# Kernel tuning notes

Hardware: AMD Instinct MI355X
Metric: run time of the kernel (lower is better)

The kernel has to match this reference:

```python
import jax, jax.numpy as jnp
import numpy as np
import math

B, S, HID = 2, 2048, 1024
NH = 16
HD = HID // NH          # 64
VD = HD // 2            # 32 value dim
TD = HD - VD            # 32 type dim
EPS = 1e-6


def setup_inputs() -> dict:
    key = jax.random.key(0)
    ks = jax.random.split(key, 12)
    std = 1.0 / math.sqrt(HID)
    xav = math.sqrt(6.0 / (TD + TD))
    return {
        "x": jax.random.normal(ks[0], (B, S, HID), dtype=jnp.float32),
        "q_w": jax.random.uniform(ks[1], (HID, HID), jnp.float32, -std, std),
        "q_b": jax.random.uniform(ks[2], (HID,), jnp.float32, -std, std),
        "k_w": jax.random.uniform(ks[3], (HID, HID), jnp.float32, -std, std),
        "k_b": jax.random.uniform(ks[4], (HID,), jnp.float32, -std, std),
        "v_w": jax.random.uniform(ks[5], (HID, HID), jnp.float32, -std, std),
        "v_b": jax.random.uniform(ks[6], (HID,), jnp.float32, -std, std),
        "out_w": jax.random.uniform(ks[7], (HID, HID), jnp.float32, -std, std),
        "out_b": jax.random.uniform(ks[8], (HID,), jnp.float32, -std, std),
        "type_bilinear": jax.random.uniform(ks[9], (NH, TD, TD), jnp.float32, -xav, xav),
        "type_bias": jnp.full((NH,), 2.0, dtype=jnp.float32),
        "mask": jnp.ones((B, S), dtype=jnp.int32),
    }


def reference(x, q_w, q_b, k_w, k_b, v_w, v_b, out_w, out_b, type_bilinear, type_bias, mask):
    # projections: [B,S,HID] -> [B,NH,S,HD]
    def proj(w, b):
        y = jnp.einsum("bsi,io->bso", x, w) + b
        return y.reshape(B, S, NH, HD).transpose(0, 2, 1, 3)

    q = proj(q_w, q_b)
    k = proj(k_w, k_b)
    v = proj(v_w, v_b)

    q_val, q_type = q[..., :VD], q[..., VD:]
    k_val, k_type = k[..., :VD], k[..., VD:]

    # standard value score: [B,NH,S,S]
    val_scores = jnp.einsum("bhqd,bhkd->bhqk", q_val, k_val) / math.sqrt(VD)

    # per-head bilinear type score: q_type @ W_h @ k_type^T + bias_h
    qt = jnp.einsum("bhqd,hde->bhqe", q_type, type_bilinear)
    type_scores = jnp.einsum("bhqe,bhke->bhqk", qt, k_type) + type_bias[None, :, None, None]
    type_unif = jax.nn.sigmoid(type_scores)

    scores = val_scores + jnp.log(type_unif + EPS)

    # mask: [B,S] -> broadcast over heads and query dim (keys masked)
    m = (mask[:, None, None, :] != 0)
    scores = jnp.where(m, scores, -jnp.inf)

    attn = jax.nn.softmax(scores, axis=-1)
    out = jnp.einsum("bhqk,bhkd->bhqd", attn, v)          # [B,NH,S,HD]
    out = out.transpose(0, 2, 1, 3).reshape(B, S, HID)
    return jnp.einsum("bsi,io->bso", out, out_w) + out_b
```

## Files before the change

### kernel.cpp

```cpp
#include <hip/hip_runtime.h>
#include <hip/hip_bf16.h>
#include <math.h>

typedef __attribute__((ext_vector_type(8))) short bf16x8;
typedef __attribute__((ext_vector_type(4))) short bf16x4;
typedef __attribute__((ext_vector_type(4))) float f32x4;
typedef __attribute__((ext_vector_type(4))) int   i32x4;

#define NHh 16
#define Sq  2048
#define HIDq 1024
#define HDq 64
#define LOG2E 1.4426950408889634f

#if __has_builtin(__builtin_amdgcn_exp2f)
#define EXP2F(x) __builtin_amdgcn_exp2f(x)
#else
#define EXP2F(x) exp2f(x)
#endif
#if __has_builtin(__builtin_amdgcn_rcpf)
#define RCPF(x) __builtin_amdgcn_rcpf(x)
#else
#define RCPF(x) (1.0f/(x))
#endif

#if __has_builtin(__builtin_amdgcn_mfma_f32_16x16x16bf16_1k)
__device__ __forceinline__ f32x4 MFMA16(bf16x4 a, bf16x4 b, f32x4 c){
  return __builtin_amdgcn_mfma_f32_16x16x16bf16_1k(a, b, c, 0, 0, 0);
}
#else
__device__ __forceinline__ f32x4 MFMA16(bf16x4 a, bf16x4 b, f32x4 c){
  asm volatile("v_mfma_f32_16x16x16_bf16 %0, %1, %2, %0\n\ts_nop 7\n\ts_nop 7"
               : "+v"(c) : "v"(a), "v"(b));
  return c;
}
#endif

__device__ __forceinline__ unsigned short f2bf(float f){
  union { float f; unsigned u; } v; v.f = f;
  unsigned r = v.u + 0x7fffu + ((v.u >> 16) & 1u);
  return (unsigned short)(r >> 16);
}
__device__ __forceinline__ float bf2f(unsigned short s){
  union { unsigned u; float f; } v; v.u = ((unsigned)s) << 16;
  return v.f;
}
__device__ __forceinline__ unsigned pk2bf(float lo, float hi){
  union { __hip_bfloat162 h; unsigned u; } w;
  w.h = __float22bfloat162_rn(make_float2(lo, hi));
  return w.u;
}

__device__ __forceinline__ void gload_lds16(const unsigned short* g, unsigned short* l){
  __builtin_amdgcn_global_load_lds(
      (const __attribute__((address_space(1))) unsigned int*)g,
      (__attribute__((address_space(3))) unsigned int*)l, 16, 0, 0);
}

__global__ __launch_bounds__(256) void convert_x(const float* __restrict__ in,
                                                 unsigned short* __restrict__ out, int n8,
                                                 const int* __restrict__ mask,
                                                 unsigned short* __restrict__ Mbf){
  int bid = blockIdx.x;
  int nmain = gridDim.x - 2;
  if (bid >= nmain){
    int base = (bid - nmain)*2048 + threadIdx.x*8;
    #pragma unroll
    for (int j=0;j<8;j++) Mbf[base+j] = mask[base+j] ? (unsigned short)0x3F80 : (unsigned short)0;
    return;
  }
  int i = bid*256 + threadIdx.x;
  if (i >= n8) return;
  const f32x4* p = (const f32x4*)(in + (size_t)i*8);
  f32x4 a = p[0], b = p[1];
  union { unsigned short us[8]; i32x4 v; } o;
  #pragma unroll
  for (int j=0;j<4;j++){ o.us[j] = f2bf(a[j]); o.us[4+j] = f2bf(b[j]); }
  *(i32x4*)(out + (size_t)i*8) = o.v;
}

__global__ __launch_bounds__(256) void transpose_w(const float* __restrict__ w0, const float* __restrict__ w1,
                                                   const float* __restrict__ w2, const float* __restrict__ w3,
                                                   unsigned short* __restrict__ wT){
  __shared__ float tile[32][33];
  int z = blockIdx.z;
  const float* w = (z==0)?w0:(z==1)?w1:(z==2)?w2:w3;
  unsigned short* dst = wT + (size_t)z*HIDq*HIDq;
  int tx = threadIdx.x, ty = threadIdx.y;
  int n0 = blockIdx.x*32, k0 = blockIdx.y*32;
  #pragma unroll
  for (int i=ty;i<32;i+=8) tile[i][tx] = w[(size_t)(k0+i)*HIDq + n0+tx];
  __syncthreads();
  #pragma unroll
  for (int i=ty;i<32;i+=8) dst[(size_t)(n0+i)*HIDq + k0+tx] = f2bf(tile[tx][i]);
}

__device__ __forceinline__ void gemm_core_gl(const unsigned short* __restrict__ Ag,
                                             const unsigned short* __restrict__ Bg,
                                             unsigned short* As, unsigned short* Bs,
                                             int t, int wv, int lane, int wr, int wc, int lr, int g,
                                             f32x4 acc[4][4]){
  for (int k0=0; k0<HIDq; k0+=64){
    __syncthreads();
    #pragma unroll
    for (int j=0;j<4;j++){
      int flat = (j*4+wv)*64 + lane;
      int row = flat>>3, c = flat&7;
      int srcc = (c ^ (row&7))*8;
      gload_lds16(Ag + (size_t)row*HIDq + k0 + srcc, &As[flat*8]);
      gload_lds16(Bg + (size_t)row*HIDq + k0 + srcc, &Bs[flat*8]);
    }
    __syncthreads();
    #pragma unroll
    for (int ks=0; ks<2; ks++){
      bf16x8 af[4], bfv[4];
      #pragma unroll
      for (int m=0;m<4;m++){
        int rr = wr + m*16 + lr;
        af[m]  = *(bf16x8*)&As[rr*64 + (((ks*4+g) ^ (rr&7))*8)];
      }
      #pragma unroll
      for (int n=0;n<4;n++){
        int rr = wc + n*16 + lr;
        bfv[n] = *(bf16x8*)&Bs[rr*64 + (((ks*4+g) ^ (rr&7))*8)];
      }
      #pragma unroll
      for (int n=0;n<4;n++)
        #pragma unroll
        for (int m=0;m<4;m++)
          acc[n][m] = __builtin_amdgcn_mfma_f32_16x16x32_bf16(bfv[n], af[m], acc[n][m], 0,0,0);
    }
  }
}

__global__ __launch_bounds__(256) void gemm_qkv(const unsigned short* __restrict__ xbf,
    const unsigned short* __restrict__ wT,
    const float* __restrict__ q_b, const float* __restrict__ k_b, const float* __restrict__ v_b,
    const int* __restrict__ mask,
    unsigned short* __restrict__ Qeff, unsigned short* __restrict__ Keff,
    unsigned short* __restrict__ Vt){
  __shared__ unsigned short As[128*64];
  __shared__ unsigned short Bs[128*64];
  const int t = threadIdx.x;
  const int wv = t>>6, lane = t&63, g = lane>>4, lr = lane&15;
  const int wr = (wv>>1)*64, wc = (wv&1)*64;
  f32x4 acc[4][4] = {};
  const int xb = blockIdx.x, yb = blockIdx.y;
  const float VS = 0.25501335f;

  if (xb < 16){
    const int row0 = yb*128, col0 = xb*128;
    gemm_core_gl(xbf + (size_t)row0*HIDq, wT + (size_t)col0*HIDq, As, Bs, t, wv, lane, wr, wc, lr, g, acc);
    #pragma unroll
    for (int n=0;n<4;n++){
      #pragma unroll
      for (int m=0;m<4;m++){
        int row = row0 + wr + m*16 + lr;
        int b_ = row>>11, ss = row&2047;
        int colb = col0 + wc + n*16 + g*4;
        int seg = colb>>10, cw = colb&1023;
        int hh = cw>>6, d = cw&63;
        const float* bp = seg ? k_b : q_b;
        f32x4 bb = *(const f32x4*)&bp[cw];
        float sc = seg ? 1.0f : (d < 32 ? VS : -LOG2E);
        unsigned short* E = seg ? Keff : Qeff;
        float v0 = (acc[n][m][0]+bb[0])*sc, v1 = (acc[n][m][1]+bb[1])*sc;
        float v2 = (acc[n][m][2]+bb[2])*sc, v3 = (acc[n][m][3]+bb[3])*sc;
        union { unsigned u[2]; unsigned long long ll; } W;
        W.u[0] = pk2bf(v0,v1); W.u[1] = pk2bf(v2,v3);
        *(unsigned long long*)&E[(((size_t)b_*NHh+hh)*Sq+ss)*HDq + d] = W.ll;
      }
    }
  } else {
    const int row0 = (xb-16)*128, col0 = yb*128;
    gemm_core_gl(wT + (size_t)2*HIDq*HIDq + (size_t)row0*HIDq, xbf + (size_t)col0*HIDq,
                 As, Bs, t, wv, lane, wr, wc, lr, g, acc);
    #pragma unroll
    for (int n=0;n<4;n++){
      #pragma unroll
      for (int m=0;m<4;m++){
        int chan = row0 + wr + m*16 + lr;
        int hh = chan>>6, d = chan&63;
        float bv = v_b[chan];
        int colb = col0 + wc + n*16 + g*4;
        int b_ = colb>>11, ss = colb&2047;
        i32x4 mk = *(const i32x4*)&mask[(size_t)b_*Sq + ss];
        float m0 = mk[0]?1.f:0.f, m1 = mk[1]?1.f:0.f, m2 = mk[2]?1.f:0.f, m3 = mk[3]?1.f:0.f;
        union { unsigned u[2]; unsigned long long ll; } W;
        W.u[0] = pk2bf((acc[n][m][0]+bv)*m0, (acc[n][m][1]+bv)*m1);
        W.u[1] = pk2bf((acc[n][m][2]+bv)*m2, (acc[n][m][3]+bv)*m3);
        *(unsigned long long*)&Vt[(((size_t)b_*NHh+hh)*HDq + d)*Sq + ss] = W.ll;
      }
    }
  }
}

__global__ __launch_bounds__(256) void gemm_out(const unsigned short* __restrict__ A,
                                                const unsigned short* __restrict__ Bt,
                                                const float* __restrict__ bias,
                                                float* __restrict__ C){
  __shared__ unsigned short As[128*64];
  __shared__ unsigned short Bs[128*64];
  const int t = threadIdx.x;
  const int wv = t>>6, lane = t&63, g = lane>>4, lr = lane&15;
  const int wr = (wv>>1)*64, wc = (wv&1)*64;
  const int row0 = blockIdx.y*128, col0 = blockIdx.x*128;
  f32x4 acc[4][4] = {};
  gemm_core_gl(A + (size_t)row0*HIDq, Bt + (size_t)col0*HIDq, As, Bs, t, wv, lane, wr, wc, lr, g, acc);
  #pragma unroll
  for (int n=0;n<4;n++){
    #pragma unroll
    for (int m=0;m<4;m++){
      int row = row0 + wr + m*16 + lr;
      int colb = col0 + wc + n*16 + g*4;
      f32x4 bb = *(const f32x4*)&bias[colb];
      f32x4 o = acc[n][m] + bb;
      *(f32x4*)&C[(size_t)row*HIDq + colb] = o;
    }
  }
}

__global__ __launch_bounds__(256,4) void attn_kernel(
    const unsigned short* __restrict__ Qe, const unsigned short* __restrict__ Ke,
    const unsigned short* __restrict__ Vt, const float* __restrict__ Tb,
    const float* __restrict__ tbias, const unsigned short* __restrict__ Mbf,
    unsigned short* __restrict__ Obuf)
{
  __shared__ __align__(16) unsigned char smem[32768];
  unsigned short* Ks0 = (unsigned short*)smem;
  unsigned short* Ks1 = (unsigned short*)(smem + 8192);
  unsigned short* Vs0 = (unsigned short*)(smem + 16384);
  unsigned short* Vs1 = (unsigned short*)(smem + 24576);
  float* qls = (float*)smem;
  unsigned short* qtls = Vs0;

  const int t = threadIdx.x;
  const int dd = blockIdx.x;
  const int slot = dd>>3, xcd = dd&7;
  const int x = slot & 31;
  const int bh = ((slot>>5)<<3) | xcd;
  const int h = bh & 15, b = bh >> 4;
  const int q0 = x*64;
  const int wv = t>>6, lane = t&63, g = lane>>4, lr = lane&15;

  const unsigned short* Qb  = Qe + (((size_t)b*NHh+h)*Sq + q0)*HDq;
  const unsigned short* Kb  = Ke + ((size_t)b*NHh+h)*(size_t)Sq*HDq;
  const unsigned short* Vtb = Vt + ((size_t)b*NHh+h)*(size_t)HDq*Sq;
  const unsigned short* Mbfb = Mbf + (size_t)b*Sq;

  {
    int row = t>>2, c8 = (t&3)*8;
    bf16x8 v = *(const bf16x8*)(Qb + (size_t)row*HDq + 32 + c8);
    #pragma unroll
    for (int j=0;j<8;j++) qls[row*33 + c8 + j] = bf2f((unsigned short)v[j]);
  }
  __syncthreads();
  {
    int row = t&63, e0 = (t>>6)*8;
    const float* Th = Tb + (size_t)h*1024;
    float a[8] = {};
    #pragma unroll 4
    for (int d=0; d<32; d++){
      float qd = qls[row*33 + d];
      const f32x4* tp = (const f32x4*)(Th + d*32 + e0);
      f32x4 t0 = tp[0], t1 = tp[1];
      a[0]+=qd*t0[0]; a[1]+=qd*t0[1]; a[2]+=qd*t0[2]; a[3]+=qd*t0[3];
      a[4]+=qd*t1[0]; a[5]+=qd*t1[1]; a[6]+=qd*t1[2]; a[7]+=qd*t1[3];
    }
    union { unsigned u[2]; unsigned long long ll; } W0, W1;
    W0.u[0]=pk2bf(a[0],a[1]); W0.u[1]=pk2bf(a[2],a[3]);
    W1.u[0]=pk2bf(a[4],a[5]); W1.u[1]=pk2bf(a[6],a[7]);
    *(unsigned long long*)&qtls[row*40 + e0]     = W0.ll;
    *(unsigned long long*)&qtls[row*40 + e0 + 4] = W1.ll;
  }
  bf16x8 qvf = *(const bf16x8*)(Qb + (size_t)(wv*16+lr)*HDq + g*8);
  __syncthreads();
  bf16x8 qtn = *(const bf16x8*)&qtls[(wv*16+lr)*40 + g*8];
  __syncthreads();

  #pragma unroll
  for (int i=0;i<2;i++){
    int c = t + i*256;
    int kr = c>>3, kc = c&7;
    gload_lds16(Kb + (size_t)kr*HDq + ((kc ^ (kr&7))*8), Ks0 + c*8);
    int vd = c>>3, vc = c&7;
    gload_lds16(Vtb + (size_t)vd*Sq + ((vc ^ (vd&7))*8), Vs0 + c*8);
  }
  __syncthreads();

  const float tbn = -tbias[h]*LOG2E;
  const f32x4 tbc = {tbn,tbn,tbn,tbn};
  const f32x4 zf = {0.f,0.f,0.f,0.f};
  f32x4 oT[4] = {};
  f32x4 lsum = {0.f,0.f,0.f,0.f};

  auto phase = [&](const unsigned short* Kc, const unsigned short* Vc, int key0,
                   bool doStage, int key0n, unsigned short* Kn, unsigned short* Vn){
    if (doStage){
      #pragma unroll
      for (int i=0;i<2;i++){
        int c = t + i*256;
        int kr = c>>3, kc = c&7;
        gload_lds16(Kb + (size_t)(key0n+kr)*HDq + ((kc ^ (kr&7))*8), Kn + c*8);
        int vd = c>>3, vc = c&7;
        gload_lds16(Vtb + (size_t)vd*Sq + key0n + ((vc ^ (vd&7))*8), Vn + c*8);
      }
    }
    f32x4 sv[4], st[4];
    __builtin_amdgcn_s_setprio(1);
    #pragma unroll
    for (int ks=0; ks<4; ks++){
      const unsigned short* kb = Kc + (ks*16+lr)*64;
      bf16x8 kf0 = *(const bf16x8*)(kb + (((g  ) ^ (lr&7))*8));
      bf16x8 kf1 = *(const bf16x8*)(kb + (((4+g) ^ (lr&7))*8));
      sv[ks] = __builtin_amdgcn_mfma_f32_16x16x32_bf16(kf0, qvf, zf, 0,0,0);
      st[ks] = __builtin_amdgcn_mfma_f32_16x16x32_bf16(kf1, qtn, tbc, 0,0,0);
    }
    __builtin_amdgcn_s_setprio(0);
    bf16x4 pa[4];
    #pragma unroll
    for (int ks=0; ks<4; ks++){
      float p0 = EXP2F(sv[ks][0]) * RCPF(1.f + EXP2F(st[ks][0]));
      float p1 = EXP2F(sv[ks][1]) * RCPF(1.f + EXP2F(st[ks][1]));
      float p2 = EXP2F(sv[ks][2]) * RCPF(1.f + EXP2F(st[ks][2]));
      float p3 = EXP2F(sv[ks][3]) * RCPF(1.f + EXP2F(st[ks][3]));
      union { unsigned u[2]; bf16x4 v; } P_;
      P_.u[0] = pk2bf(p0,p1); P_.u[1] = pk2bf(p2,p3);
      pa[ks] = P_.v;
    }
    #pragma unroll
    for (int ks=0; ks<4; ks++){
      bf16x4 mfr = *(const bf16x4*)(Mbfb + key0 + ks*16 + g*4);
      __builtin_amdgcn_s_setprio(1);
      lsum = MFMA16(pa[ks], mfr, lsum);
      #pragma unroll
      for (int db=0; db<4; db++){
        bf16x4 vf = *(const bf16x4*)(Vc + (db*16+lr)*64 + (((2*ks + (g>>1)) ^ (lr&7))*8 + 4*(g&1)));
        oT[db] = MFMA16(pa[ks], vf, oT[db]);
      }
      __builtin_amdgcn_s_setprio(0);
    }
  };

  for (int kt=0; kt<Sq; kt+=128){
    phase(Ks0, Vs0, kt,      true,           kt+64,  Ks1, Vs1);
    __syncthreads();
    phase(Ks1, Vs1, kt+64,   kt+128 < Sq,    kt+128, Ks0, Vs0);
    __syncthreads();
  }

  float linv[4];
  #pragma unroll
  for (int r=0;r<4;r++) linv[r] = (lsum[r] > 0.f) ? RCPF(lsum[r]) : 0.f;
  unsigned short* Ob = Obuf + ((size_t)b*Sq + (q0 + wv*16 + g*4))*HIDq + h*HDq + lr;
  #pragma unroll
  for (int db=0; db<4; db++){
    #pragma unroll
    for (int r=0;r<4;r++)
      Ob[(size_t)r*HIDq + db*16] = f2bf(oT[db][r]*linv[r]);
  }
}

extern "C" void kernel_launch(void* const* d_in, const int* in_sizes, int n_in,
                              void* d_out, int out_size, void* d_ws, size_t ws_size,
                              hipStream_t stream) {
  const float* x     = (const float*)d_in[0];
  const float* q_w   = (const float*)d_in[1];
  const float* q_b   = (const float*)d_in[2];
  const float* k_w   = (const float*)d_in[3];
  const float* k_b   = (const float*)d_in[4];
  const float* v_w   = (const float*)d_in[5];
  const float* v_b   = (const float*)d_in[6];
  const float* out_w = (const float*)d_in[7];
  const float* out_b = (const float*)d_in[8];
  const float* Tb    = (const float*)d_in[9];
  const float* tbias = (const float*)d_in[10];
  const int*   mask  = (const int*)d_in[11];

  const size_t MROWS = 4096;
  unsigned short* xbf  = (unsigned short*)d_ws;
  unsigned short* wT   = xbf  + MROWS*HIDq;
  unsigned short* Qeff = wT   + (size_t)4*HIDq*HIDq;
  unsigned short* Keff = Qeff + MROWS*HIDq;
  unsigned short* Vt   = Keff + MROWS*HIDq;
  unsigned short* Obuf = Vt   + MROWS*HIDq;
  unsigned short* Mbf  = Obuf + MROWS*HIDq;

  int n8 = (int)(MROWS*HIDq/8);
  convert_x<<<dim3(n8/256 + 2), dim3(256), 0, stream>>>(x, xbf, n8, mask, Mbf);
  transpose_w<<<dim3(32,32,4), dim3(32,8), 0, stream>>>(q_w, k_w, v_w, out_w, wT);

  gemm_qkv<<<dim3(24,32), dim3(256), 0, stream>>>(xbf, wT, q_b, k_b, v_b, mask, Qeff, Keff, Vt);

  attn_kernel<<<dim3(1024), dim3(256), 0, stream>>>(Qeff, Keff, Vt, Tb, tbias, Mbf, Obuf);

  gemm_out<<<dim3(8,32), dim3(256), 0, stream>>>(Obuf, wT + (size_t)3*HIDq*HIDq, out_b, (float*)d_out);
}
```

Measured before the change: 158.9 us.

## Deepen attention K/V prefetch pipeline and shrink output GEMM tiles

The attention kernel moves from a two-buffer K/V ping-pong to three K buffers and two V buffers. K is prefetched two tiles ahead and V one tile ahead, and each phase waits on an explicit vmcnt with a raw s_barrier instead of full __syncthreads. This is meant to hide global-to-LDS latency behind the MFMA work. Separately, the output GEMM switches to 128x64 tiles with its own inline k-loop, doubling the block count (16x32 grid) so more CUs are busy, at the cost of more A-tile reloads and a single-buffered loop.

```diff
diff --git a/kernel.cpp b/kernel.cpp
--- a/kernel.cpp
+++ b/kernel.cpp
@@ -200,15 +200,51 @@
                                                 const float* __restrict__ bias,
                                                 float* __restrict__ C){
   __shared__ unsigned short As[128*64];
-  __shared__ unsigned short Bs[128*64];
+  __shared__ unsigned short Bs[64*64];
   const int t = threadIdx.x;
   const int wv = t>>6, lane = t&63, g = lane>>4, lr = lane&15;
-  const int wr = (wv>>1)*64, wc = (wv&1)*64;
-  const int row0 = blockIdx.y*128, col0 = blockIdx.x*128;
-  f32x4 acc[4][4] = {};
-  gemm_core_gl(A + (size_t)row0*HIDq, Bt + (size_t)col0*HIDq, As, Bs, t, wv, lane, wr, wc, lr, g, acc);
-  #pragma unroll
-  for (int n=0;n<4;n++){
+  const int wr = (wv>>1)*64, wc = (wv&1)*32;
+  const int row0 = blockIdx.y*128, col0 = blockIdx.x*64;
+  f32x4 acc[2][4] = {};
+  for (int k0=0; k0<HIDq; k0+=64){
+    __syncthreads();
+    #pragma unroll
+    for (int j=0;j<4;j++){
+      int flat = t + j*256;
+      int row = flat>>3, c = flat&7;
+      int srcc = (c ^ (row&7))*8;
+      gload_lds16(A + (size_t)(row0+row)*HIDq + k0 + srcc, &As[flat*8]);
+    }
+    #pragma unroll
+    for (int j=0;j<2;j++){
+      int flat = t + j*256;
+      int row = flat>>3, c = flat&7;
+      int srcc = (c ^ (row&7))*8;
+      gload_lds16(Bt + (size_t)(col0+row)*HIDq + k0 + srcc, &Bs[flat*8]);
+    }
+    __syncthreads();
+    #pragma unroll
+    for (int ks=0; ks<2; ks++){
+      bf16x8 af[4], bfv[2];
+      #pragma unroll
+      for (int m=0;m<4;m++){
+        int rr = wr + m*16 + lr;
+        af[m]  = *(bf16x8*)&As[rr*64 + (((ks*4+g) ^ (rr&7))*8)];
+      }
+      #pragma unroll
+      for (int n=0;n<2;n++){
+        int rr = wc + n*16 + lr;
+        bfv[n] = *(bf16x8*)&Bs[rr*64 + (((ks*4+g) ^ (rr&7))*8)];
+      }
+      #pragma unroll
+      for (int n=0;n<2;n++)
+        #pragma unroll
+        for (int m=0;m<4;m++)
+          acc[n][m] = __builtin_amdgcn_mfma_f32_16x16x32_bf16(bfv[n], af[m], acc[n][m], 0,0,0);
+    }
+  }
+  #pragma unroll
+  for (int n=0;n<2;n++){
     #pragma unroll
     for (int m=0;m<4;m++){
       int row = row0 + wr + m*16 + lr;
@@ -226,13 +262,14 @@
     const float* __restrict__ tbias, const unsigned short* __restrict__ Mbf,
     unsigned short* __restrict__ Obuf)
 {
-  __shared__ __align__(16) unsigned char smem[32768];
-  unsigned short* Ks0 = (unsigned short*)smem;
-  unsigned short* Ks1 = (unsigned short*)(smem + 8192);
-  unsigned short* Vs0 = (unsigned short*)(smem + 16384);
-  unsigned short* Vs1 = (unsigned short*)(smem + 24576);
+  __shared__ __align__(16) unsigned char smem[40960];
+  unsigned short* Kb0 = (unsigned short*)smem;
+  unsigned short* Kb1 = (unsigned short*)(smem + 8192);
+  unsigned short* Kb2 = (unsigned short*)(smem + 16384);
+  unsigned short* Vb0 = (unsigned short*)(smem + 24576);
+  unsigned short* Vb1 = (unsigned short*)(smem + 32768);
   float* qls = (float*)smem;
-  unsigned short* qtls = Vs0;
+  unsigned short* qtls = Vb1;
 
   const int t = threadIdx.x;
   const int dd = blockIdx.x;
@@ -267,6 +304,7 @@
       a[0]+=qd*t0[0]; a[1]+=qd*t0[1]; a[2]+=qd*t0[2]; a[3]+=qd*t0[3];
       a[4]+=qd*t1[0]; a[5]+=qd*t1[1]; a[6]+=qd*t1[2]; a[7]+=qd*t1[3];
     }
+    __syncthreads();
     union { unsigned u[2]; unsigned long long ll; } W0, W1;
     W0.u[0]=pk2bf(a[0],a[1]); W0.u[1]=pk2bf(a[2],a[3]);
     W1.u[0]=pk2bf(a[4],a[5]); W1.u[1]=pk2bf(a[6],a[7]);
@@ -282,9 +320,10 @@
   for (int i=0;i<2;i++){
     int c = t + i*256;
     int kr = c>>3, kc = c&7;
-    gload_lds16(Kb + (size_t)kr*HDq + ((kc ^ (kr&7))*8), Ks0 + c*8);
+    gload_lds16(Kb + (size_t)kr*HDq + ((kc ^ (kr&7))*8), Kb0 + c*8);
     int vd = c>>3, vc = c&7;
-    gload_lds16(Vtb + (size_t)vd*Sq + ((vc ^ (vd&7))*8), Vs0 + c*8);
+    gload_lds16(Vtb + (size_t)vd*Sq + ((vc ^ (vd&7))*8), Vb0 + c*8);
+    gload_lds16(Kb + (size_t)(64+kr)*HDq + ((kc ^ (kr&7))*8), Kb1 + c*8);
   }
   __syncthreads();
 
@@ -295,17 +334,29 @@
   f32x4 lsum = {0.f,0.f,0.f,0.f};
 
   auto phase = [&](const unsigned short* Kc, const unsigned short* Vc, int key0,
-                   bool doStage, int key0n, unsigned short* Kn, unsigned short* Vn){
-    if (doStage){
+                   bool stK, int keyK, unsigned short* Kn,
+                   bool stV, int keyV, unsigned short* Vn, bool vm8){
+    if (stK){
       #pragma unroll
       for (int i=0;i<2;i++){
         int c = t + i*256;
         int kr = c>>3, kc = c&7;
-        gload_lds16(Kb + (size_t)(key0n+kr)*HDq + ((kc ^ (kr&7))*8), Kn + c*8);
+        gload_lds16(Kb + (size_t)(keyK+kr)*HDq + ((kc ^ (kr&7))*8), Kn + c*8);
+      }
+    }
+    if (stV){
+      #pragma unroll
+      for (int i=0;i<2;i++){
+        int c = t + i*256;
         int vd = c>>3, vc = c&7;
-        gload_lds16(Vtb + (size_t)vd*Sq + key0n + ((vc ^ (vd&7))*8), Vn + c*8);
-      }
-    }
+        gload_lds16(Vtb + (size_t)vd*Sq + keyV + ((vc ^ (vd&7))*8), Vn + c*8);
+      }
+    }
+    if (vm8) asm volatile("s_waitcnt vmcnt(8)" ::: "memory");
+    else     asm volatile("s_waitcnt vmcnt(4)" ::: "memory");
+    __builtin_amdgcn_sched_barrier(0);
+    __builtin_amdgcn_s_barrier();
+
     f32x4 sv[4], st[4];
     __builtin_amdgcn_s_setprio(1);
     #pragma unroll
@@ -340,14 +391,20 @@
       }
       __builtin_amdgcn_s_setprio(0);
     }
+    __builtin_amdgcn_s_barrier();
   };
 
-  for (int kt=0; kt<Sq; kt+=128){
-    phase(Ks0, Vs0, kt,      true,           kt+64,  Ks1, Vs1);
-    __syncthreads();
-    phase(Ks1, Vs1, kt+64,   kt+128 < Sq,    kt+128, Ks0, Vs0);
-    __syncthreads();
-  }
+  for (int j=0; j<5; j++){
+    int kt = j*384;
+    phase(Kb0, Vb0, kt,      true, kt+128, Kb2,  true, kt+64,  Vb1, true);
+    phase(Kb1, Vb1, kt+64,   true, kt+192, Kb0,  true, kt+128, Vb0, true);
+    phase(Kb2, Vb0, kt+128,  true, kt+256, Kb1,  true, kt+192, Vb1, true);
+    phase(Kb0, Vb1, kt+192,  true, kt+320, Kb2,  true, kt+256, Vb0, true);
+    phase(Kb1, Vb0, kt+256,  true, kt+384, Kb0,  true, kt+320, Vb1, true);
+    phase(Kb2, Vb1, kt+320,  (kt+448 < Sq), kt+448, Kb1,  true, kt+384, Vb0, true);
+  }
+  phase(Kb0, Vb0, 1920,  false, 0, Kb0,  true, 1984, Vb1, false);
+  phase(Kb1, Vb1, 1984,  false, 0, Kb0,  false, 0, Vb0,  false);
 
   float linv[4];
   #pragma unroll
@@ -394,5 +451,5 @@
 
   attn_kernel<<<dim3(1024), dim3(256), 0, stream>>>(Qeff, Keff, Vt, Tb, tbias, Mbf, Obuf);
 
-  gemm_out<<<dim3(8,32), dim3(256), 0, stream>>>(Obuf, wT + (size_t)3*HIDq*HIDq, out_b, (float*)d_out);
-}
+  gemm_out<<<dim3(16,32), dim3(256), 0, stream>>>(Obuf, wT + (size_t)3*HIDq*HIDq, out_b, (float*)d_out);
+}
```

Result: faster. 152.9 us (-3.8%).
